# Kernel optimization log

Measured on AMD Instinct MI355X. Metric: run time of the kernel, lower is better.

The kernel has to match this reference:

```python
import jax, jax.numpy as jnp
import numpy as np

B, S, C, H = 2, 4096, 640, 8
D = C // H  # head_dim = 80


def setup_inputs() -> dict:
    key = jax.random.key(0)
    ks = jax.random.split(key, 5)
    init = 0.02
    return {
        "hidden_states": jax.random.normal(ks[0], (B, S, C), dtype=jnp.float32),
        "Wq": jax.random.normal(ks[1], (C, C), dtype=jnp.float32) * init,
        "Wk": jax.random.normal(ks[2], (C, C), dtype=jnp.float32) * init,
        "Wv": jax.random.normal(ks[3], (C, C), dtype=jnp.float32) * init,
        "Wo": jax.random.normal(ks[4], (C, C), dtype=jnp.float32) * init,
        "bo": jnp.zeros((C,), dtype=jnp.float32),
    }


def reference(hidden_states, Wq, Wk, Wv, Wo, bo):
    # self-attention: encoder_hidden_states is None -> k,v from hidden_states
    x = hidden_states  # [B, S, C]
    q = jnp.einsum("bsc,cd->bsd", x, Wq)
    k = jnp.einsum("bsc,cd->bsd", x, Wk)
    v = jnp.einsum("bsc,cd->bsd", x, Wv)

    # head_to_batch_dim: [B, S, H*D] -> [B, H, S, D]
    def split_heads(t):
        return t.reshape(B, S, H, D).transpose(0, 2, 1, 3)

    q, k, v = split_heads(q), split_heads(k), split_heads(v)

    scale = 1.0 / jnp.sqrt(jnp.float32(D))
    # get_attention_scores: baddbmm(q, k^T) * scale, softmax over keys
    scores = jnp.einsum("bhqd,bhkd->bhqk", q, k) * scale  # [B, H, S, S]
    probs = jax.nn.softmax(scores, axis=-1)
    out = jnp.einsum("bhqk,bhkd->bhqd", probs, v)  # [B, H, S, D]

    # batch_to_head_dim + to_out[0] linear (Dropout is identity at eval)
    out = out.transpose(0, 2, 1, 3).reshape(B, S, C)
    out = jnp.einsum("bsc,cd->bsd", out, Wo) + bo
    # residual_connection=False, rescale_output_factor=1.0 (diffusers defaults)
    return out
```

## Files before the change

### kernel.cpp

```cpp
#include <hip/hip_runtime.h>
#include <hip/hip_bf16.h>

typedef __bf16 bf16x8 __attribute__((ext_vector_type(8)));
typedef float f32x4 __attribute__((ext_vector_type(4)));
typedef float f32x16 __attribute__((ext_vector_type(16)));
typedef unsigned short u16;
typedef unsigned int u32;
typedef u16 u16x8 __attribute__((ext_vector_type(8)));

#define DEV __device__ __forceinline__

DEV u16 f2b(float f) {
    u32 u = __builtin_bit_cast(u32, f);
    u32 r = (u + 0x7FFFu + ((u >> 16) & 1u)) >> 16;
    return (u16)r;
}
DEV bf16x8 load8(const u16* p) {
    return __builtin_bit_cast(bf16x8, *(const uint4*)p);
}
DEV u32 cvtpk(float lo, float hi) {
    u32 r;
    asm("v_cvt_pk_bf16_f32 %0, %1, %2" : "=v"(r) : "v"(lo), "v"(hi));
    return r;
}
DEV void gld_lds16(const u16* g, const char* l) {
    __builtin_amdgcn_global_load_lds(
        (const __attribute__((address_space(1))) u32*)(unsigned long long)g,
        (__attribute__((address_space(3))) u32*)(u32)(unsigned long long)l,
        16, 0, 0);
}

__global__ __launch_bounds__(256) void cvt_x(const float* __restrict__ X, u16* __restrict__ Xb) {
    long i = ((long)blockIdx.x * 256 + threadIdx.x) * 8;
    float fa[8];
    *(uint4*)fa = *(const uint4*)(X + i);
    *(uint4*)(fa + 4) = *(const uint4*)(X + i + 4);
    u16x8 t;
    #pragma unroll
    for (int j = 0; j < 8; ++j) t[j] = f2b(fa[j]);
    *(u16x8*)(Xb + i) = t;
}

__global__ __launch_bounds__(256) void cvt_w3(
    const float* __restrict__ Wq, const float* __restrict__ Wk, const float* __restrict__ Wv,
    u16* __restrict__ Wt3)
{
    const int z = blockIdx.z;
    const float* W = (z == 0) ? Wq : ((z == 1) ? Wk : Wv);
    u16* Wt = Wt3 + (long)z * 409600;
    const int k0 = blockIdx.x * 64, n0 = blockIdx.y * 64;
    const int t = threadIdx.x;
    __shared__ u16 T[64][72];
    {
        int kl = t >> 2, nc = (t & 3) * 16;
        const float* src = W + (long)(k0 + kl) * 640 + n0 + nc;
        float fa[16];
        #pragma unroll
        for (int i = 0; i < 4; ++i) *(uint4*)(fa + i * 4) = *(const uint4*)(src + i * 4);
        #pragma unroll
        for (int j = 0; j < 16; ++j) T[nc + j][kl] = f2b(fa[j]);
    }
    __syncthreads();
    {
        int nl = t >> 2, kc = (t & 3) * 16;
        u16* dst = Wt + (long)(n0 + nl) * 640 + k0 + kc;
        *(uint4*)dst = *(const uint4*)&T[nl][kc];
        *(uint4*)(dst + 8) = *(const uint4*)&T[nl][kc + 8];
    }
}
__global__ __launch_bounds__(256) void cvt_w1(const float* __restrict__ W, u16* __restrict__ Wt) {
    const int k0 = blockIdx.x * 64, n0 = blockIdx.y * 64;
    const int t = threadIdx.x;
    __shared__ u16 T[64][72];
    {
        int kl = t >> 2, nc = (t & 3) * 16;
        const float* src = W + (long)(k0 + kl) * 640 + n0 + nc;
        float fa[16];
        #pragma unroll
        for (int i = 0; i < 4; ++i) *(uint4*)(fa + i * 4) = *(const uint4*)(src + i * 4);
        #pragma unroll
        for (int j = 0; j < 16; ++j) T[nc + j][kl] = f2b(fa[j]);
    }
    __syncthreads();
    {
        int nl = t >> 2, kc = (t & 3) * 16;
        u16* dst = Wt + (long)(n0 + nl) * 640 + k0 + kc;
        *(uint4*)dst = *(const uint4*)&T[nl][kc];
        *(uint4*)(dst + 8) = *(const uint4*)&T[nl][kc + 8];
    }
}

#define GEMM_CORE(A_PTR, BT_PTR)                                                  \
    const int tid = threadIdx.x;                                                  \
    const int lane = tid & 63;                                                    \
    const int w = tid >> 6;                                                       \
    const int wm = w >> 1, wn = w & 1;                                            \
    const int lg = lane >> 4, lr = lane & 15;                                     \
    __shared__ __align__(16) char Bb[2][16384];                                   \
    auto stage = [&](int kt0, int buf) {                                          \
        _Pragma("unroll")                                                         \
        for (int i = 0; i < 4; ++i) {                                             \
            int c = i * 256 + tid;                                                \
            int n = c >> 3, cc = c & 7;                                           \
            gld_lds16(BT_PTR + (long)(n0 + n) * 640 + kt0 + ((cc ^ (n & 7)) * 8), \
                      Bb[buf] + (c & ~63) * 16);                                  \
        }                                                                         \
    };                                                                            \
    f32x4 acc[4][4] = {};                                                         \
    stage(0, 0);                                                                  \
    for (int t = 0; t < 10; ++t) {                                                \
        __syncthreads();                                                          \
        if (t < 9) stage((t + 1) * 64, (t + 1) & 1);                              \
        const char* Bc = Bb[t & 1];                                               \
        _Pragma("unroll")                                                         \
        for (int ks = 0; ks < 64; ks += 32) {                                     \
            bf16x8 a[4], b[4];                                                    \
            _Pragma("unroll")                                                     \
            for (int mi = 0; mi < 4; ++mi) {                                      \
                int row = m0 + wm * 64 + mi * 16 + lr;                            \
                a[mi] = load8(A_PTR + (long)row * 640 + t * 64 + ks + lg * 8);    \
            }                                                                     \
            _Pragma("unroll")                                                     \
            for (int ni = 0; ni < 4; ++ni) {                                      \
                int n = wn * 64 + ni * 16 + lr;                                   \
                int cc = (ks >> 3) + lg;                                          \
                b[ni] = __builtin_bit_cast(bf16x8,                                \
                    *(const uint4*)(Bc + (n * 8 + (cc ^ (n & 7))) * 16));         \
            }                                                                     \
            _Pragma("unroll")                                                     \
            for (int mi = 0; mi < 4; ++mi)                                        \
                _Pragma("unroll")                                                 \
                for (int ni = 0; ni < 4; ++ni)                                    \
                    acc[mi][ni] = __builtin_amdgcn_mfma_f32_16x16x32_bf16(        \
                        a[mi], b[ni], acc[mi][ni], 0, 0, 0);                      \
        }                                                                         \
    }

__global__ __launch_bounds__(256, 3) void gemm_qkv(
    const u16* __restrict__ X, const u16* __restrict__ Wt3,
    u16* __restrict__ q_ws, u16* __restrict__ k_ws, u16* __restrict__ v_ws)
{
    const int z = blockIdx.z;
    const u16* Wt = Wt3 + (long)z * 409600;
    const int m0 = blockIdx.x * 128;
    const int n0 = blockIdx.y * 128;
    GEMM_CORE(X, Wt)
    #pragma unroll
    for (int mi = 0; mi < 4; ++mi)
        #pragma unroll
        for (int ni = 0; ni < 4; ++ni)
            #pragma unroll
            for (int r = 0; r < 4; ++r) {
                int m = m0 + wm * 64 + mi * 16 + lg * 4 + r;
                int n = n0 + wn * 64 + ni * 16 + lr;
                int b_ = m >> 12, s = m & 4095;
                int h = n / 80, d = n % 80;
                long bh = b_ * 8 + h;
                int tt = s >> 6, jj = s & 63;
                float val = acc[mi][ni][r];
                if (z == 0) {
                    q_ws[(bh * 4096 + s) * 80 + d] = f2b(val * 0.16131517891624225f);
                } else if (z == 1) {
                    k_ws[(bh * 64 + tt) * 5120 + (((d >> 4) * 2 + ((d >> 3) & 1)) * 64 + jj) * 8 + (d & 7)] = f2b(val);
                } else {
                    int kb = jj >> 5, h2 = (jj >> 4) & 1, hv = (jj >> 2) & 1;
                    int jv = ((jj >> 3) & 1) * 4 + (jj & 3);
                    int c = kb * 2 + h2;
                    u16* vt = v_ws + (bh * 64 + tt) * 6144;
                    vt[((c * 2 + hv) * 96 + d) * 8 + jv] = f2b(val);
                    if (d == 0) vt[((c * 2 + hv) * 96 + 80) * 8 + jv] = 0x3F80;
                }
            }
}

__global__ __launch_bounds__(256, 3) void gemm_out(
    const u16* __restrict__ X, const u16* __restrict__ Wt,
    const float* __restrict__ bias, float* __restrict__ out)
{
    const int m0 = blockIdx.x * 128;
    const int n0 = blockIdx.y * 128;
    GEMM_CORE(X, Wt)
    #pragma unroll
    for (int mi = 0; mi < 4; ++mi)
        #pragma unroll
        for (int ni = 0; ni < 4; ++ni)
            #pragma unroll
            for (int r = 0; r < 4; ++r) {
                int m = m0 + wm * 64 + mi * 16 + lg * 4 + r;
                int n = n0 + wn * 64 + ni * 16 + lr;
                out[(long)m * 640 + n] = acc[mi][ni][r] + bias[n];
            }
}

__global__ __launch_bounds__(256, 2) void attn(
    const u16* __restrict__ q_ws, const u16* __restrict__ k_ws,
    const u16* __restrict__ v_ws, u16* __restrict__ o_ws)
{
    const int l = blockIdx.x;
    const int xcd = l & 7, inner = l >> 3;
    const int bh = (xcd << 1) | (inner >> 5);
    const int qx = inner & 31;
    const int qb = qx * 128;
    const int tid = threadIdx.x;
    const int lane = tid & 63;
    const int w = tid >> 6;
    const int hi = lane >> 5;
    const int lq = lane & 31;

    __shared__ __align__(16) char Vb[2][12288];

    const u16* ktile = k_ws + (long)bh * 64 * 5120;
    const u16* vtile = v_ws + (long)bh * 64 * 6144;

    bf16x8 qf[5];
    const int qrow = qb + w * 32 + lq;
    #pragma unroll
    for (int kc = 0; kc < 5; ++kc)
        qf[kc] = load8(q_ws + ((long)bh * 4096 + qrow) * 80 + kc * 16 + hi * 8);

    f32x16 acc[3] = {};

    auto stage_v = [&](int t, int buf) {
        const u16* vt_ = vtile + (long)t * 6144;
        #pragma unroll
        for (int i = 0; i < 3; ++i) {
            int c = i * 256 + tid;
            gld_lds16(vt_ + (long)c * 8, Vb[buf] + (c & ~63) * 16);
        }
    };
    auto loadK = [&](int t, bf16x8* kr) {
        const u16* kt_ = ktile + (long)t * 5120;
        #pragma unroll
        for (int kc = 0; kc < 5; ++kc)
            #pragma unroll
            for (int kb = 0; kb < 2; ++kb)
                kr[kc * 2 + kb] = load8(kt_ + (((kc * 2 + hi) * 64) + kb * 32 + lq) * 8);
    };
    auto compute = [&](const bf16x8* kr, const char* Vc) {
        f32x16 sf[2] = {};
        __builtin_amdgcn_s_setprio(1);
        #pragma unroll
        for (int kc = 0; kc < 5; ++kc)
            #pragma unroll
            for (int kb = 0; kb < 2; ++kb)
                sf[kb] = __builtin_amdgcn_mfma_f32_32x32x16_bf16(kr[kc * 2 + kb], qf[kc], sf[kb], 0, 0, 0);
        __builtin_amdgcn_s_setprio(0);
        #pragma unroll
        for (int kb = 0; kb < 2; ++kb)
            #pragma unroll
            for (int r = 0; r < 16; ++r)
                sf[kb][r] = __builtin_amdgcn_exp2f(sf[kb][r]);
        bf16x8 pa[4];
        #pragma unroll
        for (int kb = 0; kb < 2; ++kb)
            #pragma unroll
            for (int h = 0; h < 2; ++h) {
                uint4 wv;
                wv.x = cvtpk(sf[kb][h * 8 + 0], sf[kb][h * 8 + 1]);
                wv.y = cvtpk(sf[kb][h * 8 + 2], sf[kb][h * 8 + 3]);
                wv.z = cvtpk(sf[kb][h * 8 + 4], sf[kb][h * 8 + 5]);
                wv.w = cvtpk(sf[kb][h * 8 + 6], sf[kb][h * 8 + 7]);
                pa[kb * 2 + h] = __builtin_bit_cast(bf16x8, wv);
            }
        __builtin_amdgcn_s_setprio(1);
        #pragma unroll
        for (int db = 0; db < 3; ++db)
            #pragma unroll
            for (int cc = 0; cc < 4; ++cc) {
                bf16x8 vf = __builtin_bit_cast(bf16x8,
                    *(const uint4*)(Vc + ((cc * 2 + hi) * 96 + db * 32 + lq) * 16));
                acc[db] = __builtin_amdgcn_mfma_f32_32x32x16_bf16(pa[cc], vf, acc[db], 0, 0, 0);
            }
        __builtin_amdgcn_s_setprio(0);
    };

    bf16x8 kA[10], kB[10];
    loadK(0, kA);
    stage_v(0, 0);
    for (int t = 0; t < 64; t += 2) {
        __syncthreads();
        if (t < 63) stage_v(t + 1, (t + 1) & 1);
        loadK(t + 1, kB);
        compute(kA, Vb[t & 1]);
        __syncthreads();
        if (t + 1 < 63) stage_v(t + 2, t & 1);
        loadK(t + 2 < 64 ? t + 2 : 0, kA);
        compute(kB, Vb[(t + 1) & 1]);
    }

    const int b_ = bh >> 3, h8 = bh & 7;
    #pragma unroll
    for (int r = 0; r < 16; ++r) {
        int ql = (r & 3) + 8 * (r >> 2) + 4 * hi;
        float lsum = __shfl(acc[2][r], (hi << 5) + 16);
        float inv = 1.0f / lsum;
        int row = qb + w * 32 + ql;
        #pragma unroll
        for (int db = 0; db < 3; ++db) {
            int d = db * 32 + lq;
            if (d < 80)
                o_ws[((long)b_ * 4096 + row) * 640 + h8 * 80 + d] = f2b(acc[db][r] * inv);
        }
    }
}

extern "C" void kernel_launch(void* const* d_in, const int* in_sizes, int n_in,
                              void* d_out, int out_size, void* d_ws, size_t ws_size,
                              hipStream_t stream) {
    const float* x  = (const float*)d_in[0];
    const float* Wq = (const float*)d_in[1];
    const float* Wk = (const float*)d_in[2];
    const float* Wv = (const float*)d_in[3];
    const float* Wo = (const float*)d_in[4];
    const float* bo = (const float*)d_in[5];

    u16* ws = (u16*)d_ws;
    const long SZ = 5242880;
    u16* Xb   = ws;
    u16* q_ws = ws + SZ;
    u16* k_ws = ws + 2 * SZ;
    u16* v_ws = ws + 3 * SZ;
    u16* Wt3  = ws + 3 * SZ + 6291456;
    u16* o_ws = Xb;
    u16* WtO  = k_ws;

    cvt_x<<<2560, 256, 0, stream>>>(x, Xb);
    dim3 gw3(10, 10, 3);
    cvt_w3<<<gw3, 256, 0, stream>>>(Wq, Wk, Wv, Wt3);

    dim3 g1(64, 5, 3);
    gemm_qkv<<<g1, 256, 0, stream>>>(Xb, Wt3, q_ws, k_ws, v_ws);

    attn<<<512, 256, 0, stream>>>(q_ws, k_ws, v_ws, o_ws);

    dim3 gw1(10, 10);
    cvt_w1<<<gw1, 256, 0, stream>>>(Wo, WtO);
    dim3 g3(64, 5);
    gemm_out<<<g3, 256, 0, stream>>>(o_ws, WtO, bo, (float*)d_out);
}
```

Baseline: 201.7 us.

## Split attention KV range across two wave groups with LDS reduction

Doubles the attention block to 512 threads. Two groups of four waves each process half of the 64 KV tiles for the same 128 query rows, and their partial accumulators are combined through shared memory before normalization. The aim is to raise wave occupancy and latency hiding on the KV loop. In exchange it needs twice the LDS for V buffers, adds a final LDS reduction and barrier, and tightens the register budget through launch_bounds(512,4).

```diff
diff --git a/kernel.cpp b/kernel.cpp
--- a/kernel.cpp
+++ b/kernel.cpp
@@ -192,7 +192,7 @@
             }
 }
 
-__global__ __launch_bounds__(256, 2) void attn(
+__global__ __launch_bounds__(512, 4) void attn(
     const u16* __restrict__ q_ws, const u16* __restrict__ k_ws,
     const u16* __restrict__ v_ws, u16* __restrict__ o_ws)
 {
@@ -204,32 +204,36 @@
     const int tid = threadIdx.x;
     const int lane = tid & 63;
     const int w = tid >> 6;
+    const int wq = w & 3;
+    const int kvh = w >> 2;
     const int hi = lane >> 5;
     const int lq = lane & 31;
 
-    __shared__ __align__(16) char Vb[2][12288];
-
-    const u16* ktile = k_ws + (long)bh * 64 * 5120;
+    __shared__ __align__(16) char S[49152];
+
+    const u16* ktile = k_ws + (long)bh * 64 * 5120 + (long)kvh * 32 * 5120;
     const u16* vtile = v_ws + (long)bh * 64 * 6144;
 
     bf16x8 qf[5];
-    const int qrow = qb + w * 32 + lq;
+    const int qrow = qb + wq * 32 + lq;
     #pragma unroll
     for (int kc = 0; kc < 5; ++kc)
         qf[kc] = load8(q_ws + ((long)bh * 4096 + qrow) * 80 + kc * 16 + hi * 8);
 
     f32x16 acc[3] = {};
 
-    auto stage_v = [&](int t, int buf) {
-        const u16* vt_ = vtile + (long)t * 6144;
+    auto stage_v = [&](int tl, int buf) {
         #pragma unroll
         for (int i = 0; i < 3; ++i) {
-            int c = i * 256 + tid;
-            gld_lds16(vt_ + (long)c * 8, Vb[buf] + (c & ~63) * 16);
+            int c = i * 512 + tid;
+            int half = (c >= 768) ? 1 : 0;
+            int cc = c - half * 768;
+            gld_lds16(vtile + (long)(half * 32 + tl) * 6144 + (long)cc * 8,
+                      S + (half * 2 + buf) * 12288 + (cc & ~63) * 16);
         }
     };
-    auto loadK = [&](int t, bf16x8* kr) {
-        const u16* kt_ = ktile + (long)t * 5120;
+    auto loadK = [&](int tl, bf16x8* kr) {
+        const u16* kt_ = ktile + (long)tl * 5120;
         #pragma unroll
         for (int kc = 0; kc < 5; ++kc)
             #pragma unroll
@@ -277,29 +281,57 @@
     bf16x8 kA[10], kB[10];
     loadK(0, kA);
     stage_v(0, 0);
-    for (int t = 0; t < 64; t += 2) {
+    const char* Vc0 = S + (kvh * 2 + 0) * 12288;
+    const char* Vc1 = S + (kvh * 2 + 1) * 12288;
+    for (int tl = 0; tl < 32; tl += 2) {
         __syncthreads();
-        if (t < 63) stage_v(t + 1, (t + 1) & 1);
-        loadK(t + 1, kB);
-        compute(kA, Vb[t & 1]);
+        stage_v(tl + 1, 1);
+        loadK(tl + 1, kB);
+        compute(kA, Vc0);
         __syncthreads();
-        if (t + 1 < 63) stage_v(t + 2, t & 1);
-        loadK(t + 2 < 64 ? t + 2 : 0, kA);
-        compute(kB, Vb[(t + 1) & 1]);
-    }
-
-    const int b_ = bh >> 3, h8 = bh & 7;
-    #pragma unroll
-    for (int r = 0; r < 16; ++r) {
-        int ql = (r & 3) + 8 * (r >> 2) + 4 * hi;
-        float lsum = __shfl(acc[2][r], (hi << 5) + 16);
-        float inv = 1.0f / lsum;
-        int row = qb + w * 32 + ql;
-        #pragma unroll
-        for (int db = 0; db < 3; ++db) {
-            int d = db * 32 + lq;
-            if (d < 80)
-                o_ws[((long)b_ * 4096 + row) * 640 + h8 * 80 + d] = f2b(acc[db][r] * inv);
+        if (tl < 30) stage_v(tl + 2, 0);
+        loadK(tl < 30 ? tl + 2 : 0, kA);
+        compute(kB, Vc1);
+    }
+
+    __syncthreads();
+    float* comb = (float*)S;
+    const int crow = wq * 64 + lane;
+    if (kvh == 1) {
+        #pragma unroll
+        for (int db = 0; db < 3; ++db)
+            #pragma unroll
+            for (int j = 0; j < 4; ++j) {
+                f32x4 v4 = { acc[db][j * 4 + 0], acc[db][j * 4 + 1],
+                             acc[db][j * 4 + 2], acc[db][j * 4 + 3] };
+                *(f32x4*)(comb + crow * 48 + db * 16 + j * 4) = v4;
+            }
+    }
+    __syncthreads();
+    if (kvh == 0) {
+        #pragma unroll
+        for (int db = 0; db < 3; ++db)
+            #pragma unroll
+            for (int j = 0; j < 4; ++j) {
+                f32x4 v4 = *(const f32x4*)(comb + crow * 48 + db * 16 + j * 4);
+                acc[db][j * 4 + 0] += v4[0];
+                acc[db][j * 4 + 1] += v4[1];
+                acc[db][j * 4 + 2] += v4[2];
+                acc[db][j * 4 + 3] += v4[3];
+            }
+        const int b_ = bh >> 3, h8 = bh & 7;
+        #pragma unroll
+        for (int r = 0; r < 16; ++r) {
+            int ql = (r & 3) + 8 * (r >> 2) + 4 * hi;
+            float lsum = __shfl(acc[2][r], (hi << 5) + 16);
+            float inv = 1.0f / lsum;
+            int row = qb + wq * 32 + ql;
+            #pragma unroll
+            for (int db = 0; db < 3; ++db) {
+                int d = db * 32 + lq;
+                if (d < 80)
+                    o_ws[((long)b_ * 4096 + row) * 640 + h8 * 80 + d] = f2b(acc[db][r] * inv);
+            }
         }
     }
 }
@@ -331,7 +363,7 @@
     dim3 g1(64, 5, 3);
     gemm_qkv<<<g1, 256, 0, stream>>>(Xb, Wt3, q_ws, k_ws, v_ws);
 
-    attn<<<512, 256, 0, stream>>>(q_ws, k_ws, v_ws, o_ws);
+    attn<<<512, 512, 0, stream>>>(q_ws, k_ws, v_ws, o_ws);
 
     dim3 gw1(10, 10);
     cvt_w1<<<gw1, 256, 0, stream>>>(Wo, WtO);
```

Result: slower. 665.0 us (+229.8%).
